# Optimization experiments

Hardware: AMD Instinct MI355X
Metric: run time of the kernel (lower is better)

The kernel has to match this reference:

```python
import math
import jax, jax.numpy as jnp
import numpy as np

IMG_SIZE = 2048
STRIDE = 8
NUM_CLASSES = 80
TOPK = 1000
CONF_THRESH = 0.05
NMS_THRESH = 0.6
CTR_CLAMP = 32.0
SCALE_CLAMP = math.log(1000.0 / 16)
ANCHOR_SIZES = np.array([[32,32],[64,32],[32,64],[64,64],[128,64],[64,128],[128,128],[256,128],[128,256]], dtype=np.float32)


def make_anchors():
    fmp = IMG_SIZE // STRIDE  # 256
    yy, xx = np.meshgrid(np.arange(fmp), np.arange(fmp), indexing='ij')
    xy = (np.stack([xx, yy], axis=-1).reshape(-1, 2).astype(np.float32) + 0.5) * STRIDE  # [fmp*fmp, 2]
    na = ANCHOR_SIZES.shape[0]
    xy = np.repeat(xy[:, None, :], na, axis=1)           # [fmp*fmp, na, 2]
    wh = np.tile(ANCHOR_SIZES[None, :, :], (fmp * fmp, 1, 1))  # [fmp*fmp, na, 2]
    return jnp.asarray(np.concatenate([xy, wh], axis=-1).reshape(-1, 4))  # [M, 4]


def setup_inputs() -> dict:
    key = jax.random.key(0)
    k1, k2 = jax.random.split(key)
    M = (IMG_SIZE // STRIDE) ** 2 * ANCHOR_SIZES.shape[0]
    cls_pred = jax.random.normal(k1, (M, NUM_CLASSES), dtype=jnp.float32) * 2.0 - 2.0
    reg_pred = jax.random.normal(k2, (M, 4), dtype=jnp.float32) * 0.5
    anchor_boxes = make_anchors()
    return {"cls_pred": cls_pred, "reg_pred": reg_pred, "anchor_boxes": anchor_boxes}


def decode_boxes(anchors, reg):
    # anchors, reg: [N, 4] (cx, cy, w, h) / (dx, dy, dw, dh)
    ctr_off = jnp.clip(reg[..., :2] * anchors[..., 2:], -CTR_CLAMP, CTR_CLAMP)
    ctr = anchors[..., :2] + ctr_off
    wh = anchors[..., 2:] * jnp.exp(jnp.minimum(reg[..., 2:], SCALE_CLAMP))
    return jnp.concatenate([ctr - 0.5 * wh, ctr + 0.5 * wh], axis=-1)


def iou_matrix(boxes):
    # boxes: [N, 4] x1y1x2y2 -> [N, N] IoU, matching the numpy NMS math
    x1, y1, x2, y2 = boxes[:, 0], boxes[:, 1], boxes[:, 2], boxes[:, 3]
    areas = (x2 - x1) * (y2 - y1)
    xx1 = jnp.maximum(x1[:, None], x1[None, :])
    yy1 = jnp.maximum(y1[:, None], y1[None, :])
    xx2 = jnp.minimum(x2[:, None], x2[None, :])
    yy2 = jnp.minimum(y2[:, None], y2[None, :])
    w = jnp.maximum(1e-10, xx2 - xx1)
    h = jnp.maximum(1e-10, yy2 - yy1)
    inter = w * h
    return inter / (areas[:, None] + areas[None, :] - inter + 1e-10)


def reference(cls_pred, reg_pred, anchor_boxes):
    # per-anchor best class score/label
    probs = jax.nn.sigmoid(cls_pred)                 # [M, C]
    scores_all = jnp.max(probs, axis=-1)             # [M]
    labels_all = jnp.argmax(probs, axis=-1)          # [M]
    # top-k filtering (scores sorted descending)
    scores, idx = jax.lax.top_k(scores_all, TOPK)    # [K]
    labels = labels_all[idx]
    reg = reg_pred[idx]
    anch = anchor_boxes[idx]
    # decode + normalize
    bboxes = jnp.clip(decode_boxes(anch, reg) / IMG_SIZE, 0.0, 1.0)  # [K, 4]
    valid = scores >= CONF_THRESH                    # conf filter as mask (fixed shape)
    # per-class greedy NMS: candidates are score-sorted, so greedy order = index order
    iou = iou_matrix(bboxes)                         # [K, K]
    same_cls = labels[:, None] == labels[None, :]    # [K, K]
    suppress_mat = (iou > NMS_THRESH) & same_cls     # j suppresses i if kept, same class, earlier
    idx_range = jnp.arange(TOPK)

    def body(i, keep):
        earlier_kept_overlap = jnp.any(keep & suppress_mat[:, i] & (idx_range < i))
        return keep.at[i].set(valid[i] & ~earlier_kept_overlap)

    keep = jax.lax.fori_loop(0, TOPK, body, jnp.zeros(TOPK, dtype=bool))
    return bboxes, scores, labels, keep
```

## Files before the change

### kernel.cpp

```cpp
#include <hip/hip_runtime.h>
#include <math.h>

#define M_ANCH   589824
#define NCLS     80
#define TOPK_N   1000
#define CAND_CAP 4096
#define NREP     16
#define NBIN     8192
#define KSHIFT   19

#define SCALE_CLAMP_F 4.135166556742356f
#define INV_IMG       (1.0f/2048.0f)

#define WS_H1R     0
#define WS_CNT     524288
#define WS_GBIN    524292
#define WS_MEMSET  524296
#define WS_CAND    524544
#define WS_BOXES   557312
#define WS_LABELS  573312
#define WS_VALID   577312
#define WS_SUP     581376
#define WS_MKEYS   709632

__device__ __forceinline__ unsigned fmap(unsigned b) {
    return (b & 0x80000000u) ? ~b : (b | 0x80000000u);
}
__device__ __forceinline__ unsigned funmap(unsigned k) {
    return (k & 0x80000000u) ? (k ^ 0x80000000u) : ~k;
}

__global__ __launch_bounds__(256) void k_rowmax(const float* __restrict__ cls,
                                                unsigned* __restrict__ mkeys,
                                                unsigned* __restrict__ h1r) {
    __shared__ unsigned lh[NBIN];
    int t = threadIdx.x;
    for (int b = t; b < NBIN; b += 256) lh[b] = 0;
    __syncthreads();
    int lane = t & 63, w = t >> 6;
    int part = lane & 3;
    int rsub = (w << 4) + (lane >> 2);
#pragma unroll
    for (int it = 0; it < 4; ++it) {
        int row = blockIdx.x * 256 + it * 64 + rsub;
        const float4* p = (const float4*)(cls + (size_t)row * NCLS) + part * 5;
        float m = -INFINITY;
#pragma unroll
        for (int i = 0; i < 5; ++i) {
            float4 v = p[i];
            m = fmaxf(m, fmaxf(fmaxf(v.x, v.y), fmaxf(v.z, v.w)));
        }
        m = fmaxf(m, __shfl_xor(m, 1));
        m = fmaxf(m, __shfl_xor(m, 2));
        if (part == 0) {
            unsigned key = fmap(__float_as_uint(m));
            mkeys[row] = key;
            atomicAdd(&lh[key >> KSHIFT], 1u);
        }
    }
    __syncthreads();
    unsigned rep = (blockIdx.x & (NREP - 1)) * NBIN;
    for (int b = t; b < NBIN; b += 256) {
        unsigned c = lh[b];
        if (c) atomicAdd(&h1r[rep + b], c);
    }
}

__global__ __launch_bounds__(1024) void k_find(const unsigned* __restrict__ h1r,
                                               unsigned* __restrict__ gbin) {
    __shared__ unsigned hist[NBIN];
    __shared__ unsigned csum[256];
    int t = threadIdx.x;
    for (int b = t; b < NBIN; b += 1024) {
        unsigned s = 0;
#pragma unroll
        for (int r = 0; r < NREP; ++r) s += h1r[r * NBIN + b];
        hist[b] = s;
    }
    __syncthreads();
    if (t < 256) {
        unsigned cs = 0;
        for (int k = 0; k < 32; ++k) cs += hist[t * 32 + k];
        csum[t] = cs;
    }
    __syncthreads();
    if (t == 0) {
        unsigned cum = 0, above = 0;
        int C = 0;
        for (int c = 255; c >= 0; --c) {
            if (cum + csum[c] >= TOPK_N || c == 0) { C = c; above = cum; break; }
            cum += csum[c];
        }
        int B = C * 32;
        unsigned cum2 = above;
        for (int b = C * 32 + 31; b >= C * 32; --b) {
            cum2 += hist[b];
            if (cum2 >= TOPK_N) { B = b; break; }
            if (b == C * 32) B = b;
        }
        *gbin = (B >= 1) ? (unsigned)(B - 1) : 0u;
    }
}

__global__ __launch_bounds__(256) void k_gather(const uint4* __restrict__ mk4,
                                                const unsigned* __restrict__ gbin,
                                                unsigned* __restrict__ cnt,
                                                unsigned long long* __restrict__ cand) {
    int tid = blockIdx.x * 256 + threadIdx.x;
    unsigned gb = *gbin;
    uint4 a = mk4[tid * 2];
    uint4 b4 = mk4[tid * 2 + 1];
    unsigned keys[8] = {a.x, a.y, a.z, a.w, b4.x, b4.y, b4.z, b4.w};
    int lc = 0;
    unsigned sel[8];
#pragma unroll
    for (int q = 0; q < 8; ++q)
        if ((keys[q] >> KSHIFT) >= gb) sel[lc++] = (unsigned)q;
    if (lc) {
        unsigned base = atomicAdd(cnt, (unsigned)lc);
        for (int q = 0; q < lc; ++q) {
            unsigned pos = base + (unsigned)q;
            if (pos < CAND_CAP) {
                unsigned i = (unsigned)tid * 8u + sel[q];
                float m = __uint_as_float(funmap(keys[sel[q]]));
                float e = (float)exp(-(double)m);
                float sc = 1.0f / (1.0f + e);
                cand[pos] = ((unsigned long long)__float_as_uint(sc) << 32)
                            | (unsigned)(~i);
            }
        }
    }
}

__global__ __launch_bounds__(256) void k_rank_decode(const unsigned* __restrict__ cnt,
                                                     const unsigned long long* __restrict__ cand,
                                                     const float* __restrict__ cls,
                                                     const float* __restrict__ reg,
                                                     const float* __restrict__ anch,
                                                     float* __restrict__ out,
                                                     float4* __restrict__ boxes_ws,
                                                     int* __restrict__ lab_ws,
                                                     int* __restrict__ val_ws) {
    __shared__ unsigned long long sh[CAND_CAP];
    int t = threadIdx.x;
    unsigned n = *cnt;
    if (n > CAND_CAP) n = CAND_CAP;
    for (int k = t; k < (int)n; k += 256) sh[k] = cand[k];
    __syncthreads();
    int k = blockIdx.x * 256 + t;
    if (k >= (int)n) return;
    unsigned long long key = sh[k];
    int rank = 0;
    for (int j = 0; j < (int)n; ++j) rank += (sh[j] > key) ? 1 : 0;
    if (rank >= TOPK_N) return;
    int r = rank;
    unsigned idx = ~(unsigned)(key & 0xFFFFFFFFull);
    float sc = __uint_as_float((unsigned)(key >> 32));
    const float* row = cls + (size_t)idx * NCLS;
    float best = -INFINITY;
    int lbl = 0;
    for (int c = 0; c < NCLS; ++c) {
        float v = row[c];
        if (v > best) { best = v; lbl = c; }
    }
    float4 rg = ((const float4*)reg)[idx];
    float4 an = ((const float4*)anch)[idx];
    float ox = fminf(fmaxf(rg.x * an.z, -32.0f), 32.0f);
    float oy = fminf(fmaxf(rg.y * an.w, -32.0f), 32.0f);
    float cx = an.x + ox, cy = an.y + oy;
    float w = an.z * expf(fminf(rg.z, SCALE_CLAMP_F));
    float h = an.w * expf(fminf(rg.w, SCALE_CLAMP_F));
    float x1 = fminf(fmaxf((cx - 0.5f * w) * INV_IMG, 0.0f), 1.0f);
    float y1 = fminf(fmaxf((cy - 0.5f * h) * INV_IMG, 0.0f), 1.0f);
    float x2 = fminf(fmaxf((cx + 0.5f * w) * INV_IMG, 0.0f), 1.0f);
    float y2 = fminf(fmaxf((cy + 0.5f * h) * INV_IMG, 0.0f), 1.0f);
    out[r * 4 + 0] = x1;
    out[r * 4 + 1] = y1;
    out[r * 4 + 2] = x2;
    out[r * 4 + 3] = y2;
    out[4 * TOPK_N + r] = sc;
    out[5 * TOPK_N + r] = (float)lbl;
    boxes_ws[r] = make_float4(x1, y1, x2, y2);
    lab_ws[r] = lbl;
    val_ws[r] = (sc >= 0.05f) ? 1 : 0;
}

__global__ __launch_bounds__(64) void k_sup(const float4* __restrict__ boxes,
                                            const int* __restrict__ labs,
                                            unsigned long long* __restrict__ sup) {
    int i = blockIdx.x;
    int lane = threadIdx.x;
    int cmax = i >> 6;
    float4 bi = boxes[i];
    float ai = (bi.z - bi.x) * (bi.w - bi.y);
    int li = labs[i];
    for (int c = 0; c <= cmax; ++c) {
        int j = c * 64 + lane;
        bool bit = false;
        if (j < TOPK_N) {
            float4 bj = boxes[j];
            float aj = (bj.z - bj.x) * (bj.w - bj.y);
            float xx1 = fmaxf(bi.x, bj.x), yy1 = fmaxf(bi.y, bj.y);
            float xx2 = fminf(bi.z, bj.z), yy2 = fminf(bi.w, bj.w);
            float w = fmaxf(1e-10f, xx2 - xx1);
            float h = fmaxf(1e-10f, yy2 - yy1);
            float inter = w * h;
            float iou = inter / (ai + aj - inter + 1e-10f);
            bit = (iou > 0.6f) && (labs[j] == li);
        }
        unsigned long long ball = __ballot(bit);
        if (lane == 0) sup[(size_t)i * 16 + c] = ball;
    }
}

__global__ __launch_bounds__(64) void k_nms(const unsigned long long* __restrict__ sup,
                                            const int* __restrict__ val,
                                            float* __restrict__ out_keep) {
    int lane = threadIdx.x;
    unsigned long long kw[16];
#pragma unroll
    for (int c = 0; c < 16; ++c) kw[c] = 0ull;
    unsigned long long lowmask = (lane == 0) ? 0ull : (~0ull >> (64 - lane));
    for (int c = 0; c < 16; ++c) {
        int b = c * 64 + lane;
        bool v = false;
        bool ext = false;
        unsigned long long m = 0ull;
        if (b < TOPK_N) {
            v = (val[b] != 0);
            const unsigned long long* rowp = sup + (size_t)b * 16;
            for (int w = 0; w < c; ++w) ext = ext || ((rowp[w] & kw[w]) != 0ull);
            m = rowp[c];
        }
        unsigned long long inchunk = m & lowmask;
        bool mykeep;
        if (__ballot(inchunk != 0ull) == 0ull) {
            mykeep = v && !ext;
        } else {
            mykeep = false;
            for (int i = 0; i < 64; ++i) {
                unsigned long long ball = __ballot(mykeep);
                if (lane == i) mykeep = v && !ext && ((ball & inchunk) == 0ull);
            }
        }
        unsigned long long ball2 = __ballot(mykeep);
        kw[c] = ball2;
        if (b < TOPK_N) out_keep[b] = ((ball2 >> lane) & 1ull) ? 1.0f : 0.0f;
    }
}

extern "C" void kernel_launch(void* const* d_in, const int* in_sizes, int n_in,
                              void* d_out, int out_size, void* d_ws, size_t ws_size,
                              hipStream_t stream) {
    const float* cls  = (const float*)d_in[0];
    const float* reg  = (const float*)d_in[1];
    const float* anch = (const float*)d_in[2];
    float* out = (float*)d_out;
    char* ws = (char*)d_ws;

    unsigned* h1r  = (unsigned*)(ws + WS_H1R);
    unsigned* cnt  = (unsigned*)(ws + WS_CNT);
    unsigned* gbin = (unsigned*)(ws + WS_GBIN);
    unsigned long long* cand = (unsigned long long*)(ws + WS_CAND);
    float4* boxes = (float4*)(ws + WS_BOXES);
    int* labs     = (int*)(ws + WS_LABELS);
    int* valid    = (int*)(ws + WS_VALID);
    unsigned long long* sup = (unsigned long long*)(ws + WS_SUP);
    unsigned* mkeys = (unsigned*)(ws + WS_MKEYS);

    hipMemsetAsync(ws, 0, WS_MEMSET, stream);

    k_rowmax<<<M_ANCH / 256, 256, 0, stream>>>(cls, mkeys, h1r);
    k_find  <<<1, 1024, 0, stream>>>(h1r, gbin);
    k_gather<<<M_ANCH / (256 * 8), 256, 0, stream>>>((const uint4*)mkeys, gbin, cnt, cand);
    k_rank_decode<<<CAND_CAP / 256, 256, 0, stream>>>(cnt, cand, cls, reg, anch,
                                                      out, boxes, labs, valid);
    k_sup   <<<TOPK_N, 64, 0, stream>>>(boxes, labs, sup);
    k_nms   <<<1, 64, 0, stream>>>(sup, valid, out + 6 * TOPK_N);
}
```

Baseline: 386.1 us.

## Fuse rank/decode, suppression matrix and NMS into one single-block tail kernel

Merges the rank-decode, pairwise suppression and greedy NMS kernels into one 1024-thread block. Boxes, labels and valid flags now stay in shared memory instead of going through global workspace, which removes two kernel launches and the global round-trips between them. The row-max kernel also interleaves its float4 loads across the four lanes so adjacent lanes read adjacent vectors. The cost is that rank, decode and the IoU matrix now run on a single CU instead of many blocks, so that work is serialized more.

```diff
diff --git a/kernel.cpp b/kernel.cpp
--- a/kernel.cpp
+++ b/kernel.cpp
@@ -17,9 +17,6 @@
 #define WS_GBIN    524292
 #define WS_MEMSET  524296
 #define WS_CAND    524544
-#define WS_BOXES   557312
-#define WS_LABELS  573312
-#define WS_VALID   577312
 #define WS_SUP     581376
 #define WS_MKEYS   709632
 
@@ -43,11 +40,11 @@
 #pragma unroll
     for (int it = 0; it < 4; ++it) {
         int row = blockIdx.x * 256 + it * 64 + rsub;
-        const float4* p = (const float4*)(cls + (size_t)row * NCLS) + part * 5;
+        const float4* p = (const float4*)(cls + (size_t)row * NCLS);
         float m = -INFINITY;
 #pragma unroll
         for (int i = 0; i < 5; ++i) {
-            float4 v = p[i];
+            float4 v = p[i * 4 + part];
             m = fmaxf(m, fmaxf(fmaxf(v.x, v.y), fmaxf(v.z, v.w)));
         }
         m = fmaxf(m, __shfl_xor(m, 1));
@@ -132,120 +129,144 @@
     }
 }
 
-__global__ __launch_bounds__(256) void k_rank_decode(const unsigned* __restrict__ cnt,
-                                                     const unsigned long long* __restrict__ cand,
-                                                     const float* __restrict__ cls,
-                                                     const float* __restrict__ reg,
-                                                     const float* __restrict__ anch,
-                                                     float* __restrict__ out,
-                                                     float4* __restrict__ boxes_ws,
-                                                     int* __restrict__ lab_ws,
-                                                     int* __restrict__ val_ws) {
+__global__ __launch_bounds__(1024) void k_tail(const unsigned* __restrict__ cnt,
+                                               const unsigned long long* __restrict__ cand,
+                                               const float* __restrict__ cls,
+                                               const float* __restrict__ reg,
+                                               const float* __restrict__ anch,
+                                               float* __restrict__ out,
+                                               unsigned long long* __restrict__ sup) {
     __shared__ unsigned long long sh[CAND_CAP];
+    __shared__ float4 sboxes[TOPK_N];
+    __shared__ int    slab[TOPK_N];
+    __shared__ int    sval[TOPK_N];
     int t = threadIdx.x;
     unsigned n = *cnt;
     if (n > CAND_CAP) n = CAND_CAP;
-    for (int k = t; k < (int)n; k += 256) sh[k] = cand[k];
-    __syncthreads();
-    int k = blockIdx.x * 256 + t;
-    if (k >= (int)n) return;
-    unsigned long long key = sh[k];
-    int rank = 0;
-    for (int j = 0; j < (int)n; ++j) rank += (sh[j] > key) ? 1 : 0;
-    if (rank >= TOPK_N) return;
-    int r = rank;
-    unsigned idx = ~(unsigned)(key & 0xFFFFFFFFull);
-    float sc = __uint_as_float((unsigned)(key >> 32));
-    const float* row = cls + (size_t)idx * NCLS;
-    float best = -INFINITY;
-    int lbl = 0;
-    for (int c = 0; c < NCLS; ++c) {
-        float v = row[c];
-        if (v > best) { best = v; lbl = c; }
-    }
-    float4 rg = ((const float4*)reg)[idx];
-    float4 an = ((const float4*)anch)[idx];
-    float ox = fminf(fmaxf(rg.x * an.z, -32.0f), 32.0f);
-    float oy = fminf(fmaxf(rg.y * an.w, -32.0f), 32.0f);
-    float cx = an.x + ox, cy = an.y + oy;
-    float w = an.z * expf(fminf(rg.z, SCALE_CLAMP_F));
-    float h = an.w * expf(fminf(rg.w, SCALE_CLAMP_F));
-    float x1 = fminf(fmaxf((cx - 0.5f * w) * INV_IMG, 0.0f), 1.0f);
-    float y1 = fminf(fmaxf((cy - 0.5f * h) * INV_IMG, 0.0f), 1.0f);
-    float x2 = fminf(fmaxf((cx + 0.5f * w) * INV_IMG, 0.0f), 1.0f);
-    float y2 = fminf(fmaxf((cy + 0.5f * h) * INV_IMG, 0.0f), 1.0f);
-    out[r * 4 + 0] = x1;
-    out[r * 4 + 1] = y1;
-    out[r * 4 + 2] = x2;
-    out[r * 4 + 3] = y2;
-    out[4 * TOPK_N + r] = sc;
-    out[5 * TOPK_N + r] = (float)lbl;
-    boxes_ws[r] = make_float4(x1, y1, x2, y2);
-    lab_ws[r] = lbl;
-    val_ws[r] = (sc >= 0.05f) ? 1 : 0;
-}
-
-__global__ __launch_bounds__(64) void k_sup(const float4* __restrict__ boxes,
-                                            const int* __restrict__ labs,
-                                            unsigned long long* __restrict__ sup) {
-    int i = blockIdx.x;
-    int lane = threadIdx.x;
-    int cmax = i >> 6;
-    float4 bi = boxes[i];
-    float ai = (bi.z - bi.x) * (bi.w - bi.y);
-    int li = labs[i];
-    for (int c = 0; c <= cmax; ++c) {
-        int j = c * 64 + lane;
-        bool bit = false;
-        if (j < TOPK_N) {
-            float4 bj = boxes[j];
-            float aj = (bj.z - bj.x) * (bj.w - bj.y);
-            float xx1 = fmaxf(bi.x, bj.x), yy1 = fmaxf(bi.y, bj.y);
-            float xx2 = fminf(bi.z, bj.z), yy2 = fminf(bi.w, bj.w);
-            float w = fmaxf(1e-10f, xx2 - xx1);
-            float h = fmaxf(1e-10f, yy2 - yy1);
-            float inter = w * h;
-            float iou = inter / (ai + aj - inter + 1e-10f);
-            bit = (iou > 0.6f) && (labs[j] == li);
-        }
-        unsigned long long ball = __ballot(bit);
-        if (lane == 0) sup[(size_t)i * 16 + c] = ball;
-    }
-}
-
-__global__ __launch_bounds__(64) void k_nms(const unsigned long long* __restrict__ sup,
-                                            const int* __restrict__ val,
-                                            float* __restrict__ out_keep) {
-    int lane = threadIdx.x;
-    unsigned long long kw[16];
-#pragma unroll
-    for (int c = 0; c < 16; ++c) kw[c] = 0ull;
-    unsigned long long lowmask = (lane == 0) ? 0ull : (~0ull >> (64 - lane));
-    for (int c = 0; c < 16; ++c) {
-        int b = c * 64 + lane;
-        bool v = false;
-        bool ext = false;
-        unsigned long long m = 0ull;
-        if (b < TOPK_N) {
-            v = (val[b] != 0);
-            const unsigned long long* rowp = sup + (size_t)b * 16;
-            for (int w = 0; w < c; ++w) ext = ext || ((rowp[w] & kw[w]) != 0ull);
-            m = rowp[c];
-        }
-        unsigned long long inchunk = m & lowmask;
-        bool mykeep;
-        if (__ballot(inchunk != 0ull) == 0ull) {
-            mykeep = v && !ext;
-        } else {
-            mykeep = false;
-            for (int i = 0; i < 64; ++i) {
-                unsigned long long ball = __ballot(mykeep);
-                if (lane == i) mykeep = v && !ext && ((ball & inchunk) == 0ull);
-            }
-        }
-        unsigned long long ball2 = __ballot(mykeep);
-        kw[c] = ball2;
-        if (b < TOPK_N) out_keep[b] = ((ball2 >> lane) & 1ull) ? 1.0f : 0.0f;
+    for (int k = t; k < (int)n; k += 1024) sh[k] = cand[k];
+    __syncthreads();
+
+    unsigned long long kk0 = (t          < (int)n) ? sh[t]          : 0ull;
+    unsigned long long kk1 = (t + 1024   < (int)n) ? sh[t + 1024]   : 0ull;
+    unsigned long long kk2 = (t + 2048   < (int)n) ? sh[t + 2048]   : 0ull;
+    unsigned long long kk3 = (t + 3072   < (int)n) ? sh[t + 3072]   : 0ull;
+    int r0 = 0, r1 = 0, r2 = 0, r3 = 0;
+    int j = 0;
+    for (; j + 1 < (int)n; j += 2) {
+        unsigned long long v0 = sh[j], v1 = sh[j + 1];
+        r0 += (v0 > kk0) + (v1 > kk0);
+        r1 += (v0 > kk1) + (v1 > kk1);
+        r2 += (v0 > kk2) + (v1 > kk2);
+        r3 += (v0 > kk3) + (v1 > kk3);
+    }
+    for (; j < (int)n; ++j) {
+        unsigned long long v0 = sh[j];
+        r0 += (v0 > kk0); r1 += (v0 > kk1); r2 += (v0 > kk2); r3 += (v0 > kk3);
+    }
+
+    int   rks[4] = {r0, r1, r2, r3};
+    unsigned long long kks[4] = {kk0, kk1, kk2, kk3};
+#pragma unroll
+    for (int q = 0; q < 4; ++q) {
+        int k = t + 1024 * q;
+        if (k >= (int)n) continue;
+        int r = rks[q];
+        if (r >= TOPK_N) continue;
+        unsigned long long key = kks[q];
+        unsigned idx = ~(unsigned)(key & 0xFFFFFFFFull);
+        float sc = __uint_as_float((unsigned)(key >> 32));
+        const float4* rowp = (const float4*)(cls + (size_t)idx * NCLS);
+        float best = -INFINITY;
+        int lbl = 0;
+#pragma unroll
+        for (int c4 = 0; c4 < 20; ++c4) {
+            float4 v = rowp[c4];
+            if (v.x > best) { best = v.x; lbl = c4 * 4; }
+            if (v.y > best) { best = v.y; lbl = c4 * 4 + 1; }
+            if (v.z > best) { best = v.z; lbl = c4 * 4 + 2; }
+            if (v.w > best) { best = v.w; lbl = c4 * 4 + 3; }
+        }
+        float4 rg = ((const float4*)reg)[idx];
+        float4 an = ((const float4*)anch)[idx];
+        float ox = fminf(fmaxf(rg.x * an.z, -32.0f), 32.0f);
+        float oy = fminf(fmaxf(rg.y * an.w, -32.0f), 32.0f);
+        float cx = an.x + ox, cy = an.y + oy;
+        float w = an.z * expf(fminf(rg.z, SCALE_CLAMP_F));
+        float h = an.w * expf(fminf(rg.w, SCALE_CLAMP_F));
+        float x1 = fminf(fmaxf((cx - 0.5f * w) * INV_IMG, 0.0f), 1.0f);
+        float y1 = fminf(fmaxf((cy - 0.5f * h) * INV_IMG, 0.0f), 1.0f);
+        float x2 = fminf(fmaxf((cx + 0.5f * w) * INV_IMG, 0.0f), 1.0f);
+        float y2 = fminf(fmaxf((cy + 0.5f * h) * INV_IMG, 0.0f), 1.0f);
+        out[r * 4 + 0] = x1;
+        out[r * 4 + 1] = y1;
+        out[r * 4 + 2] = x2;
+        out[r * 4 + 3] = y2;
+        out[4 * TOPK_N + r] = sc;
+        out[5 * TOPK_N + r] = (float)lbl;
+        sboxes[r] = make_float4(x1, y1, x2, y2);
+        slab[r] = lbl;
+        sval[r] = (sc >= 0.05f) ? 1 : 0;
+    }
+    __syncthreads();
+
+    int wid = t >> 6, lane = t & 63;
+    for (int i = wid; i < TOPK_N; i += 16) {
+        float4 bi = sboxes[i];
+        float ai = (bi.z - bi.x) * (bi.w - bi.y);
+        int li = slab[i];
+        int cmax = i >> 6;
+        for (int c = 0; c <= cmax; ++c) {
+            int jj = c * 64 + lane;
+            bool bit = false;
+            if (jj < TOPK_N) {
+                float4 bj = sboxes[jj];
+                float aj = (bj.z - bj.x) * (bj.w - bj.y);
+                float xx1 = fmaxf(bi.x, bj.x), yy1 = fmaxf(bi.y, bj.y);
+                float xx2 = fminf(bi.z, bj.z), yy2 = fminf(bi.w, bj.w);
+                float w = fmaxf(1e-10f, xx2 - xx1);
+                float h = fmaxf(1e-10f, yy2 - yy1);
+                float inter = w * h;
+                float iou = inter / (ai + aj - inter + 1e-10f);
+                bit = (iou > 0.6f) && (slab[jj] == li);
+            }
+            unsigned long long ball = __ballot(bit);
+            if (lane == 0) sup[(size_t)i * 16 + c] = ball;
+        }
+    }
+    __syncthreads();
+
+    if (t < 64) {
+        float* out_keep = out + 6 * TOPK_N;
+        unsigned long long kw[16];
+#pragma unroll
+        for (int c = 0; c < 16; ++c) kw[c] = 0ull;
+        unsigned long long lowmask = (lane == 0) ? 0ull : (~0ull >> (64 - lane));
+        for (int c = 0; c < 16; ++c) {
+            int b = c * 64 + lane;
+            bool v = false;
+            bool ext = false;
+            unsigned long long m = 0ull;
+            if (b < TOPK_N) {
+                v = (sval[b] != 0);
+                const unsigned long long* rowp = sup + (size_t)b * 16;
+                for (int w = 0; w < c; ++w) ext = ext || ((rowp[w] & kw[w]) != 0ull);
+                m = rowp[c];
+            }
+            unsigned long long inchunk = m & lowmask;
+            bool mykeep;
+            if (__ballot(inchunk != 0ull) == 0ull) {
+                mykeep = v && !ext;
+            } else {
+                mykeep = false;
+                for (int i = 0; i < 64; ++i) {
+                    unsigned long long ball = __ballot(mykeep);
+                    if (lane == i) mykeep = v && !ext && ((ball & inchunk) == 0ull);
+                }
+            }
+            unsigned long long ball2 = __ballot(mykeep);
+            kw[c] = ball2;
+            if (b < TOPK_N) out_keep[b] = ((ball2 >> lane) & 1ull) ? 1.0f : 0.0f;
+        }
     }
 }
 
@@ -262,9 +283,6 @@
     unsigned* cnt  = (unsigned*)(ws + WS_CNT);
     unsigned* gbin = (unsigned*)(ws + WS_GBIN);
     unsigned long long* cand = (unsigned long long*)(ws + WS_CAND);
-    float4* boxes = (float4*)(ws + WS_BOXES);
-    int* labs     = (int*)(ws + WS_LABELS);
-    int* valid    = (int*)(ws + WS_VALID);
     unsigned long long* sup = (unsigned long long*)(ws + WS_SUP);
     unsigned* mkeys = (unsigned*)(ws + WS_MKEYS);
 
@@ -273,8 +291,5 @@
     k_rowmax<<<M_ANCH / 256, 256, 0, stream>>>(cls, mkeys, h1r);
     k_find  <<<1, 1024, 0, stream>>>(h1r, gbin);
     k_gather<<<M_ANCH / (256 * 8), 256, 0, stream>>>((const uint4*)mkeys, gbin, cnt, cand);
-    k_rank_decode<<<CAND_CAP / 256, 256, 0, stream>>>(cnt, cand, cls, reg, anch,
-                                                      out, boxes, labs, valid);
-    k_sup   <<<TOPK_N, 64, 0, stream>>>(boxes, labs, sup);
-    k_nms   <<<1, 64, 0, stream>>>(sup, valid, out + 6 * TOPK_N);
-}
+    k_tail  <<<1, 1024, 0, stream>>>(cnt, cand, cls, reg, anch, out, sup);
+}
```

After: 659.1 us. +70.7%, slower.
